# Kernel optimization log

Hardware: AMD Instinct MI355X
Metric: run time of the kernel (lower is better)

The kernel has to match this reference:

```python
import jax, jax.numpy as jnp
import numpy as np

B, T, IN, H, C = 128, 128, 75, 512, 60


def setup_inputs() -> dict:
    key = jax.random.key(0)
    ks = jax.random.split(key, 40)
    def n(k, shape, s=0.05):
        return jax.random.normal(k, shape, dtype=jnp.float32) * s
    p = {}
    p["inputs"] = jax.random.normal(ks[0], (B, T, IN), dtype=jnp.float32)
    p["epoch"] = 1
    # three used LSTMCells: lstm_cell_t, lstm_cell (spatial), lstm_cell1
    i = 1
    for nm, isz in [("t", IN), ("s", IN), ("1", IN)]:
        p[f"Wih_{nm}"] = n(ks[i], (4 * H, isz)); i += 1
        p[f"Whh_{nm}"] = n(ks[i], (4 * H, H)); i += 1
        p[f"bih_{nm}"] = n(ks[i], (4 * H,)); i += 1
        p[f"bhh_{nm}"] = n(ks[i], (4 * H,)); i += 1
    p["fc_w"] = n(ks[i], (C, H)); i += 1
    p["fc_b"] = n(ks[i], (C,)); i += 1
    p["fct_w"] = n(ks[i], (H, IN)); i += 1
    p["fct_b"] = n(ks[i], (H,)); i += 1
    p["fc1_w"] = n(ks[i], (H, IN)); i += 1
    p["fc1_b"] = n(ks[i], (H,)); i += 1
    p["fc2_w"] = n(ks[i], (IN // 3, H)); i += 1
    p["fc2_b"] = n(ks[i], (IN // 3,)); i += 1
    p["W_x_t"] = n(ks[i], (H, H)); i += 1
    p["W_h_t"] = n(ks[i], (H, H)); i += 1
    p["b_t"] = n(ks[i], (H,)); i += 1
    p["W_x_s"] = n(ks[i], (H, H)); i += 1
    p["W_h_s"] = n(ks[i], (H, H)); i += 1
    p["U_s"] = n(ks[i], (H, H)); i += 1
    p["b_s"] = n(ks[i], (H,)); i += 1
    p["b_us"] = n(ks[i], (H,)); i += 1
    return p


def reference(inputs, epoch,
              Wih_t, Whh_t, bih_t, bhh_t,
              Wih_s, Whh_s, bih_s, bhh_s,
              Wih_1, Whh_1, bih_1, bhh_1,
              fc_w, fc_b, fct_w, fct_b, fc1_w, fc1_b, fc2_w, fc2_b,
              W_x_t, W_h_t, b_t, W_x_s, W_h_s, U_s, b_s, b_us):
    def cell(x, h, c, Wih, Whh, bih, bhh):
        g = x @ Wih.T + bih + h @ Whh.T + bhh            # [B, 4H]
        i, f, gg, o = jnp.split(g, 4, axis=1)
        c2 = jax.nn.sigmoid(f) * c + jax.nn.sigmoid(i) * jnp.tanh(gg)
        return jax.nn.sigmoid(o) * jnp.tanh(c2), c2

    def step(carry, x):  # x: [B, IN]
        hn_t, cn_t, hn_s, cn_s, hn1, cn1 = carry
        h_prev_t = hn_t
        hn_t, cn_t = cell(x, hn_t, cn_t, Wih_t, Whh_t, bih_t, bhh_t)
        # temporal gate beta (note: original adds BOTH b_s and b_t)
        beta = jax.nn.relu((x @ fct_w.T + fct_b) @ W_x_t + h_prev_t @ W_h_t + b_s + b_t)
        h_prev = hn_s
        hn_s, cn_s = cell(x, hn_s, cn_s, Wih_s, Whh_s, bih_s, bhh_s)
        st = jnp.tanh((x @ fc1_w.T + fc1_b) @ W_x_s + h_prev @ W_h_s + b_s)
        st = st @ U_s + b_us
        q = st @ fc2_w.T + fc2_b                          # [B, IN/3]
        alpha = jax.nn.softmax(q, axis=1)                  # exp(q)/sum(exp(q))
        x_gated = x * jnp.repeat(alpha, 3, axis=1)
        hn1, cn1 = cell(x_gated, hn1, cn1, Wih_1, Whh_1, bih_1, bhh_1)
        # torch in-place aliasing bug: zt = hn1; zt *= beta mutates hn1,
        # so the gated value is carried as the next-step hidden state.
        hn1 = hn1 * beta
        return (hn_t, cn_t, hn_s, cn_s, hn1, cn1), (hn1, alpha, beta)

    Bn, Tn = inputs.shape[0], inputs.shape[1]
    z = jnp.zeros((Bn, Whh_t.shape[1]), dtype=inputs.dtype)
    init = (z, z, z, z, z, z)
    xs = jnp.swapaxes(inputs, 0, 1)  # [T, B, IN]
    _, (outs, alphas, betas) = jax.lax.scan(step, init, xs)
    logits = outs[-1] @ fc_w.T + fc_b
    logp = jax.nn.log_softmax(logits, axis=-1)
    # original reshapes the [T, B, *] stacks directly to (B, T, -1)
    alpha_out = alphas.reshape(Bn, Tn, -1)
    beta_out = betas.reshape(Bn, Tn, -1)
    return logp, alpha_out, beta_out
```

## Files before the change

kernel.cpp:

```cpp
#include <hip/hip_runtime.h>
#include <math.h>

#define B_ 128
#define T_ 128
#define IN_ 75
#define H_ 512
#define C_ 60
#define Q_ 25

constexpr size_t OFF_WHHP = 0;
constexpr size_t OFF_WIHP = 6291456;
constexpr size_t OFF_WXHP = 7225344;
constexpr size_t OFF_FT2P = 9322496;
constexpr size_t OFF_U2   = 9478144;
constexpr size_t OFF_B2   = 9529344;
constexpr size_t OFF_XP   = 9529472;
constexpr size_t OFF_HT2  = 12019840;
constexpr size_t OFF_HS2  = 12281984;
constexpr size_t OFF_T12  = 12544128;
constexpr size_t OFF_T22  = 12806272;
constexpr size_t OFF_H12  = 13068416;
constexpr size_t OFF_CT   = 13199488;
constexpr size_t OFF_CS   = 13461632;
constexpr size_t OFF_C1   = 13723776;
constexpr size_t OFF_G1H  = 13985920;
constexpr size_t OFF_ST   = 14510208;
constexpr size_t OFF_BETA = 14772352;
constexpr size_t WS_BYTES = 15034496;

struct Full {
  const float* inputs;
  const float* Wih_t; const float* Whh_t; const float* bih_t; const float* bhh_t;
  const float* Wih_s; const float* Whh_s; const float* bih_s; const float* bhh_s;
  const float* Wih_1; const float* Whh_1; const float* bih_1; const float* bhh_1;
  const float* fc_w;  const float* fc_b;
  const float* fct_w; const float* fct_b;
  const float* fc1_w; const float* fc1_b;
  const float* fc2_w; const float* fc2_b;
  const float* W_x_t; const float* W_h_t; const float* b_t;
  const float* W_x_s; const float* W_h_s; const float* U_s; const float* b_s; const float* b_us;
  char* ws; float* out;
};

typedef _Float16 h2t __attribute__((ext_vector_type(2)));
union U32H { unsigned u; h2t h; unsigned short s[2]; };

__device__ __forceinline__ float sigm(float v) { return 1.f / (1.f + expf(-v)); }
__device__ __forceinline__ float dot2(unsigned a, unsigned b, float c) {
#if __has_builtin(__builtin_amdgcn_fdot2)
  U32H A, B; A.u = a; B.u = b;
  return __builtin_amdgcn_fdot2(A.h, B.h, c, false);
#else
  U32H A, B; A.u = a; B.u = b;
  return fmaf((float)A.h.x, (float)B.h.x, fmaf((float)A.h.y, (float)B.h.y, c));
#endif
}
__device__ __forceinline__ unsigned pack2h(float a, float b) {
  U32H r; r.h.x = (_Float16)a; r.h.y = (_Float16)b; return r.u;
}
__device__ __forceinline__ float hlo(unsigned v) { U32H r; r.u = v; return (float)r.h.x; }
__device__ __forceinline__ float hhi(unsigned v) { U32H r; r.u = v; return (float)r.h.y; }

__global__ void prep_pack(Full f) {
  uint4* WHHP = (uint4*)(f.ws + OFF_WHHP);
  uint4* WIHP = (uint4*)(f.ws + OFF_WIHP);
  unsigned* WXHP = (unsigned*)(f.ws + OFF_WXHP);
  unsigned* FT2P = (unsigned*)(f.ws + OFF_FT2P);
  float* U2 = (float*)(f.ws + OFF_U2);
  float* B2 = (float*)(f.ws + OFF_B2);
  unsigned* XP = (unsigned*)(f.ws + OFF_XP);

  const size_t N1 = (size_t)3 * 256 * 512;
  const size_t N2 = (size_t)3 * 38 * 512;
  const size_t N3 = (size_t)4 * 256 * 512;
  const size_t N4 = (size_t)2 * 38 * 512;
  const size_t N5 = (size_t)25 * 512;
  const size_t N6 = 25;
  const size_t N7 = (size_t)128 * 38 * 128;
  const size_t TOT = N1 + N2 + N3 + N4 + N5 + N6 + N7;
  for (size_t i = (size_t)blockIdx.x * blockDim.x + threadIdx.x; i < TOT;
       i += (size_t)gridDim.x * blockDim.x) {
    if (i < N1) {
      size_t c = i / 131072, r = i % 131072, k2 = r >> 9, u = r & 511;
      const float* W = (c == 0) ? f.Whh_t : (c == 1) ? f.Whh_s : f.Whh_1;
      uint4 v;
      v.x = pack2h(W[(0 * 512 + u) * 512 + 2 * k2], W[(0 * 512 + u) * 512 + 2 * k2 + 1]);
      v.y = pack2h(W[(1 * 512 + u) * 512 + 2 * k2], W[(1 * 512 + u) * 512 + 2 * k2 + 1]);
      v.z = pack2h(W[(2 * 512 + u) * 512 + 2 * k2], W[(2 * 512 + u) * 512 + 2 * k2 + 1]);
      v.w = pack2h(W[(3 * 512 + u) * 512 + 2 * k2], W[(3 * 512 + u) * 512 + 2 * k2 + 1]);
      WHHP[i] = v;
    } else if (i < N1 + N2) {
      size_t e = i - N1; size_t c = e / 19456, r = e % 19456, k2 = r >> 9, u = r & 511;
      const float* W = (c == 0) ? f.Wih_t : (c == 1) ? f.Wih_s : f.Wih_1;
      int k = 2 * (int)k2;
      uint4 v;
#pragma unroll
      for (int g = 0; g < 4; ++g) {
        float a = (k < 75) ? W[(g * 512 + u) * 75 + k] : 0.f;
        float b = (k + 1 < 75) ? W[(g * 512 + u) * 75 + k + 1] : 0.f;
        (&v.x)[g] = pack2h(a, b);
      }
      WIHP[e] = v;
    } else if (i < N1 + N2 + N3) {
      size_t e = i - N1 - N2; size_t w = e / 131072, r = e % 131072, k2 = r >> 9, u = r & 511;
      const float* W = (w == 0) ? f.W_x_t : (w == 1) ? f.W_h_t : (w == 2) ? f.W_x_s : f.W_h_s;
      WXHP[e] = pack2h(W[2 * k2 * 512 + u], W[(2 * k2 + 1) * 512 + u]);
    } else if (i < N1 + N2 + N3 + N4) {
      size_t e = i - N1 - N2 - N3; size_t c = e / 19456, r = e % 19456, k2 = r >> 9, u = r & 511;
      const float* W = c ? f.fc1_w : f.fct_w;
      int k = 2 * (int)k2;
      float a = (k < 75) ? W[u * 75 + k] : 0.f;
      float b = (k + 1 < 75) ? W[u * 75 + k + 1] : 0.f;
      FT2P[e] = pack2h(a, b);
    } else if (i < N1 + N2 + N3 + N4 + N5) {
      size_t e = i - N1 - N2 - N3 - N4; size_t qi = e >> 9, u = e & 511;
      float acc = 0.f;
      for (int n = 0; n < 512; ++n) acc = fmaf(f.U_s[u * 512 + n], f.fc2_w[qi * 512 + n], acc);
      U2[qi * 512 + u] = acc;
    } else if (i < N1 + N2 + N3 + N4 + N5 + N6) {
      size_t qi = i - N1 - N2 - N3 - N4 - N5;
      float acc = f.fc2_b[qi];
      for (int n = 0; n < 512; ++n) acc = fmaf(f.b_us[n], f.fc2_w[qi * 512 + n], acc);
      B2[qi] = acc;
    } else {
      size_t e = i - N1 - N2 - N3 - N4 - N5 - N6;
      size_t t = e / 4864, r = e % 4864, k2 = r >> 7, b = r & 127;
      int k = 2 * (int)k2;
      const size_t base = ((size_t)b * T_ + t) * IN_;
      float xa = (k < 75) ? f.inputs[base + k] : 0.f;
      float xb = (k + 1 < 75) ? f.inputs[base + k + 1] : 0.f;
      XP[e] = pack2h(xa, xb);
    }
  }
}

__global__ __launch_bounds__(512) void prep_state(Full f) {
  const int b = blockIdx.x, j = threadIdx.x;
  __shared__ float x0[77];
  __shared__ float t1L[512], t2L[512];
  if (j < IN_) x0[j] = f.inputs[(size_t)b * T_ * IN_ + j];
  __syncthreads();
  float t1 = f.fct_b[j], t2 = f.fc1_b[j];
  for (int k = 0; k < IN_; ++k) {
    t1 = fmaf(x0[k], f.fct_w[j * IN_ + k], t1);
    t2 = fmaf(x0[k], f.fc1_w[j * IN_ + k], t2);
  }
  t1L[j] = t1; t2L[j] = t2;
  __syncthreads();
  ((float*)(f.ws + OFF_CT))[(size_t)j * 128 + b] = 0.f;
  ((float*)(f.ws + OFF_CS))[(size_t)j * 128 + b] = 0.f;
  ((float*)(f.ws + OFF_C1))[(size_t)j * 128 + b] = 0.f;
  if (j < 256) {
    ((unsigned*)(f.ws + OFF_HT2))[(size_t)j * 128 + b] = 0u;
    ((unsigned*)(f.ws + OFF_HS2))[(size_t)j * 128 + b] = 0u;
    ((unsigned*)(f.ws + OFF_H12))[(size_t)j * 128 + b] = 0u;
    ((unsigned*)(f.ws + OFF_T12))[(size_t)j * 128 + b] = pack2h(t1L[2 * j], t1L[2 * j + 1]);
    ((unsigned*)(f.ws + OFF_T22))[(size_t)j * 128 + b] = pack2h(t2L[2 * j], t2L[2 * j + 1]);
  }
}

__global__ __launch_bounds__(256) void k1(Full f, int t) {
  const int tid = threadIdx.x, bid = blockIdx.x;
  const int row = tid & 127, half = tid >> 7;
  const int cur = t & 1;

  char* wsb = f.ws;
  const uint4* WHHP = (const uint4*)(wsb + OFF_WHHP);
  const uint4* WIHP = (const uint4*)(wsb + OFF_WIHP);
  const unsigned* WXHP = (const unsigned*)(wsb + OFF_WXHP);
  const unsigned* FT2P = (const unsigned*)(wsb + OFF_FT2P);
  const unsigned* XP = (const unsigned*)(wsb + OFF_XP);
  unsigned* HT2 = (unsigned*)(wsb + OFF_HT2);
  unsigned* HS2 = (unsigned*)(wsb + OFF_HS2);
  unsigned* T12 = (unsigned*)(wsb + OFF_T12);
  unsigned* T22 = (unsigned*)(wsb + OFF_T22);
  unsigned* H12 = (unsigned*)(wsb + OFF_H12);
  float* CT = (float*)(wsb + OFF_CT);
  float* CS = (float*)(wsb + OFF_CS);
  uint4* G1H = (uint4*)(wsb + OFF_G1H);
  float* ST = (float*)(wsb + OFF_ST);
  float* BETA = (float*)(wsb + OFF_BETA);
  float* out_beta = f.out + B_ * C_ + (size_t)T_ * B_ * Q_;

  if (bid < 384) {
    const int c = bid / 128;
    const int up = (bid % 128) * 2 + half;
    const int u0 = 2 * up, u1 = u0 + 1;
    const unsigned* Sr = (c == 0) ? (HT2 + (size_t)cur * 32768)
                       : (c == 1) ? (HS2 + (size_t)cur * 32768) : H12;
    float a0 = 0, a1 = 0, a2 = 0, a3 = 0, a4 = 0, a5 = 0, a6 = 0, a7 = 0;
#pragma unroll 4
    for (int k2 = 0; k2 < 256; ++k2) {
      const unsigned s = Sr[k2 * 128 + row];
      const uint4 w0 = WHHP[((size_t)(c * 256 + k2) << 9) + u0];
      const uint4 w1 = WHHP[((size_t)(c * 256 + k2) << 9) + u1];
      a0 = dot2(s, w0.x, a0); a1 = dot2(s, w0.y, a1);
      a2 = dot2(s, w0.z, a2); a3 = dot2(s, w0.w, a3);
      a4 = dot2(s, w1.x, a4); a5 = dot2(s, w1.y, a5);
      a6 = dot2(s, w1.z, a6); a7 = dot2(s, w1.w, a7);
    }
    if (c < 2) {
#pragma unroll 2
      for (int k2 = 0; k2 < 38; ++k2) {
        const unsigned xp = XP[((size_t)t * 38 + k2) * 128 + row];
        const uint4 w0 = WIHP[((size_t)(c * 38 + k2) << 9) + u0];
        const uint4 w1 = WIHP[((size_t)(c * 38 + k2) << 9) + u1];
        a0 = dot2(xp, w0.x, a0); a1 = dot2(xp, w0.y, a1);
        a2 = dot2(xp, w0.z, a2); a3 = dot2(xp, w0.w, a3);
        a4 = dot2(xp, w1.x, a4); a5 = dot2(xp, w1.y, a5);
        a6 = dot2(xp, w1.z, a6); a7 = dot2(xp, w1.w, a7);
      }
      const float* bi = c ? f.bih_s : f.bih_t;
      const float* bh = c ? f.bhh_s : f.bhh_t;
      float* Cst = c ? CS : CT;
      float h0, h1v;
      {
        const float iv = sigm(a0 + bi[u0] + bh[u0]);
        const float fv = sigm(a1 + bi[512 + u0] + bh[512 + u0]);
        const float gv = tanhf(a2 + bi[1024 + u0] + bh[1024 + u0]);
        const float ov = sigm(a3 + bi[1536 + u0] + bh[1536 + u0]);
        const float cc = fv * Cst[(size_t)u0 * 128 + row] + iv * gv;
        Cst[(size_t)u0 * 128 + row] = cc;
        h0 = ov * tanhf(cc);
      }
      {
        const float iv = sigm(a4 + bi[u1] + bh[u1]);
        const float fv = sigm(a5 + bi[512 + u1] + bh[512 + u1]);
        const float gv = tanhf(a6 + bi[1024 + u1] + bh[1024 + u1]);
        const float ov = sigm(a7 + bi[1536 + u1] + bh[1536 + u1]);
        const float cc = fv * Cst[(size_t)u1 * 128 + row] + iv * gv;
        Cst[(size_t)u1 * 128 + row] = cc;
        h1v = ov * tanhf(cc);
      }
      unsigned* Sw = (c ? HS2 : HT2) + (size_t)(cur ^ 1) * 32768;
      Sw[up * 128 + row] = pack2h(h0, h1v);
    } else {
      uint4 g;
      g.x = pack2h(a0 + f.bih_1[u0] + f.bhh_1[u0], a4 + f.bih_1[u1] + f.bhh_1[u1]);
      g.y = pack2h(a1 + f.bih_1[512 + u0] + f.bhh_1[512 + u0],
                   a5 + f.bih_1[512 + u1] + f.bhh_1[512 + u1]);
      g.z = pack2h(a2 + f.bih_1[1024 + u0] + f.bhh_1[1024 + u0],
                   a6 + f.bih_1[1024 + u1] + f.bhh_1[1024 + u1]);
      g.w = pack2h(a3 + f.bih_1[1536 + u0] + f.bhh_1[1536 + u0],
                   a7 + f.bih_1[1536 + u1] + f.bhh_1[1536 + u1]);
      G1H[(size_t)up * 128 + row] = g;
    }
  } else if (bid < 512) {
    const int up = (bid - 384) * 2 + half;
    const int u0 = 2 * up, u1 = u0 + 1;
    const unsigned* T1r = T12 + (size_t)cur * 32768;
    const unsigned* HTr = HT2 + (size_t)cur * 32768;
    float aB0 = 0, aB1 = 0;
#pragma unroll 4
    for (int k2 = 0; k2 < 256; ++k2) {
      const unsigned t1 = T1r[k2 * 128 + row];
      const unsigned ht = HTr[k2 * 128 + row];
      aB0 = dot2(t1, WXHP[((size_t)k2 << 9) + u0], aB0);
      aB0 = dot2(ht, WXHP[((size_t)(256 + k2) << 9) + u0], aB0);
      aB1 = dot2(t1, WXHP[((size_t)k2 << 9) + u1], aB1);
      aB1 = dot2(ht, WXHP[((size_t)(256 + k2) << 9) + u1], aB1);
    }
    {
      const float bv = fmaxf(aB0 + f.b_s[u0] + f.b_t[u0], 0.f);
      BETA[(size_t)u0 * 128 + row] = bv;
      out_beta[((size_t)t * B_ + row) * H_ + u0] = bv;
    }
    {
      const float bv = fmaxf(aB1 + f.b_s[u1] + f.b_t[u1], 0.f);
      BETA[(size_t)u1 * 128 + row] = bv;
      out_beta[((size_t)t * B_ + row) * H_ + u1] = bv;
    }
    if (t < T_ - 1) {
      float tn0 = 0, tn1 = 0;
#pragma unroll 2
      for (int k2 = 0; k2 < 38; ++k2) {
        const unsigned xp = XP[((size_t)(t + 1) * 38 + k2) * 128 + row];
        tn0 = dot2(xp, FT2P[((size_t)k2 << 9) + u0], tn0);
        tn1 = dot2(xp, FT2P[((size_t)k2 << 9) + u1], tn1);
      }
      T12[(size_t)(cur ^ 1) * 32768 + up * 128 + row] =
          pack2h(tn0 + f.fct_b[u0], tn1 + f.fct_b[u1]);
    }
  } else {
    const int up = (bid - 512) * 2 + half;
    const int u0 = 2 * up, u1 = u0 + 1;
    const unsigned* T2r = T22 + (size_t)cur * 32768;
    const unsigned* HSr = HS2 + (size_t)cur * 32768;
    float aS0 = 0, aS1 = 0;
#pragma unroll 4
    for (int k2 = 0; k2 < 256; ++k2) {
      const unsigned t2 = T2r[k2 * 128 + row];
      const unsigned hs = HSr[k2 * 128 + row];
      aS0 = dot2(t2, WXHP[((size_t)(512 + k2) << 9) + u0], aS0);
      aS0 = dot2(hs, WXHP[((size_t)(768 + k2) << 9) + u0], aS0);
      aS1 = dot2(t2, WXHP[((size_t)(512 + k2) << 9) + u1], aS1);
      aS1 = dot2(hs, WXHP[((size_t)(768 + k2) << 9) + u1], aS1);
    }
    ST[(size_t)u0 * 128 + row] = tanhf(aS0 + f.b_s[u0]);
    ST[(size_t)u1 * 128 + row] = tanhf(aS1 + f.b_s[u1]);
    if (t < T_ - 1) {
      float tn0 = 0, tn1 = 0;
#pragma unroll 2
      for (int k2 = 0; k2 < 38; ++k2) {
        const unsigned xp = XP[((size_t)(t + 1) * 38 + k2) * 128 + row];
        tn0 = dot2(xp, FT2P[((size_t)(38 + k2) << 9) + u0], tn0);
        tn1 = dot2(xp, FT2P[((size_t)(38 + k2) << 9) + u1], tn1);
      }
      T22[(size_t)(cur ^ 1) * 32768 + up * 128 + row] =
          pack2h(tn0 + f.fc1_b[u0], tn1 + f.fc1_b[u1]);
    }
  }
}

__global__ __launch_bounds__(256) void k2(Full f, int t) {
  const int tid = threadIdx.x, row = blockIdx.x;
  char* wsb = f.ws;
  const uint4* WIHP = (const uint4*)(wsb + OFF_WIHP);
  const float* U2 = (const float*)(wsb + OFF_U2);
  const float* B2 = (const float*)(wsb + OFF_B2);
  const float* ST = (const float*)(wsb + OFF_ST);
  const float* BETA = (const float*)(wsb + OFF_BETA);
  const uint4* G1H = (const uint4*)(wsb + OFF_G1H);
  float* C1 = (float*)(wsb + OFF_C1);
  unsigned* H12 = (unsigned*)(wsb + OFF_H12);
  float* out_alpha = f.out + B_ * C_;

  __shared__ float stv[512];
  __shared__ float qp[200];
  __shared__ float qv[25];
  __shared__ float al[25];
  __shared__ unsigned xgp[40];

  stv[tid] = ST[(size_t)tid * 128 + row];
  stv[tid + 256] = ST[(size_t)(tid + 256) * 128 + row];
  __syncthreads();
  if (tid < 200) {
    const int qi = tid >> 3, ks = tid & 7;
    const float* u2p = U2 + (size_t)qi * 512 + ks * 64;
    const float* sp = stv + ks * 64;
    float acc = 0.f;
    for (int j = 0; j < 64; j += 4) {
      const float4 uv = *(const float4*)(u2p + j);
      const float4 sv = *(const float4*)(sp + j);
      acc += sv.x * uv.x + sv.y * uv.y + sv.z * uv.z + sv.w * uv.w;
    }
    qp[tid] = acc;
  }
  __syncthreads();
  if (tid < 25) {
    float s = B2[tid];
    for (int j = 0; j < 8; ++j) s += qp[tid * 8 + j];
    qv[tid] = s;
  }
  __syncthreads();
  if (tid < 25) {
    float m = qv[0];
    for (int i2 = 1; i2 < 25; ++i2) m = fmaxf(m, qv[i2]);
    float s = 0.f;
    for (int i2 = 0; i2 < 25; ++i2) s += expf(qv[i2] - m);
    const float a = expf(qv[tid] - m) / s;
    al[tid] = a;
    out_alpha[((size_t)t * B_ + row) * Q_ + tid] = a;
  }
  __syncthreads();
  if (tid < 38) {
    const int k = 2 * tid;
    const size_t base = ((size_t)row * T_ + t) * IN_;
    const float xa = f.inputs[base + k] * al[k / 3];
    const float xb = (k + 1 < IN_) ? f.inputs[base + k + 1] * al[(k + 1) / 3] : 0.f;
    xgp[tid] = pack2h(xa, xb);
  }
  __syncthreads();
  const int u0 = 2 * tid, u1 = u0 + 1;
  float c0 = 0, c1a = 0, c2 = 0, c3 = 0, c4 = 0, c5 = 0, c6 = 0, c7 = 0;
#pragma unroll 2
  for (int k2 = 0; k2 < 38; ++k2) {
    const unsigned xp = xgp[k2];
    const uint4 w0 = WIHP[((size_t)(2 * 38 + k2) << 9) + u0];
    const uint4 w1 = WIHP[((size_t)(2 * 38 + k2) << 9) + u1];
    c0 = dot2(xp, w0.x, c0); c1a = dot2(xp, w0.y, c1a);
    c2 = dot2(xp, w0.z, c2); c3 = dot2(xp, w0.w, c3);
    c4 = dot2(xp, w1.x, c4); c5 = dot2(xp, w1.y, c5);
    c6 = dot2(xp, w1.z, c6); c7 = dot2(xp, w1.w, c7);
  }
  const uint4 g = G1H[(size_t)tid * 128 + row];
  float h0, h1v;
  {
    const float i1 = sigm(c0 + hlo(g.x)), f1 = sigm(c1a + hlo(g.y));
    const float gg = tanhf(c2 + hlo(g.z)), o1 = sigm(c3 + hlo(g.w));
    const float cc = f1 * C1[(size_t)u0 * 128 + row] + i1 * gg;
    C1[(size_t)u0 * 128 + row] = cc;
    h0 = o1 * tanhf(cc) * BETA[(size_t)u0 * 128 + row];
  }
  {
    const float i1 = sigm(c4 + hhi(g.x)), f1 = sigm(c5 + hhi(g.y));
    const float gg = tanhf(c6 + hhi(g.z)), o1 = sigm(c7 + hhi(g.w));
    const float cc = f1 * C1[(size_t)u1 * 128 + row] + i1 * gg;
    C1[(size_t)u1 * 128 + row] = cc;
    h1v = o1 * tanhf(cc) * BETA[(size_t)u1 * 128 + row];
  }
  H12[(size_t)tid * 128 + row] = pack2h(h0, h1v);
}

__global__ __launch_bounds__(256) void k3(Full f) {
  const int tid = threadIdx.x, row = blockIdx.x;
  const unsigned* H12 = (const unsigned*)(f.ws + OFF_H12);
  __shared__ float hv[512];
  __shared__ float part[240];
  __shared__ float lg[60];
  {
    const unsigned v = H12[(size_t)tid * 128 + row];
    hv[2 * tid] = hlo(v);
    hv[2 * tid + 1] = hhi(v);
  }
  __syncthreads();
  if (tid < 240) {
    const int ci = tid >> 2, ks = tid & 3;
    const float* fr = f.fc_w + (size_t)ci * 512 + ks * 128;
    const float* hr = hv + ks * 128;
    float acc = 0.f;
    for (int j = 0; j < 128; j += 4) {
      const float4 fv = *(const float4*)(fr + j);
      const float4 hq = *(const float4*)(hr + j);
      acc += hq.x * fv.x + hq.y * fv.y + hq.z * fv.z + hq.w * fv.w;
    }
    part[tid] = acc;
  }
  __syncthreads();
  if (tid < 60) {
    float s = f.fc_b[tid];
    for (int j = 0; j < 4; ++j) s += part[tid * 4 + j];
    lg[tid] = s;
  }
  __syncthreads();
  if (tid < 60) {
    float m = lg[0];
    for (int i2 = 1; i2 < 60; ++i2) m = fmaxf(m, lg[i2]);
    float ssum = 0.f;
    for (int i2 = 0; i2 < 60; ++i2) ssum += expf(lg[i2] - m);
    f.out[(size_t)row * C_ + tid] = lg[tid] - m - logf(ssum);
  }
}

extern "C" void kernel_launch(void* const* d_in, const int* in_sizes, int n_in,
                              void* d_out, int out_size, void* d_ws, size_t ws_size,
                              hipStream_t stream) {
  if (ws_size < WS_BYTES) return;

  Full f;
  f.inputs = (const float*)d_in[0];
  f.Wih_t = (const float*)d_in[2];  f.Whh_t = (const float*)d_in[3];
  f.bih_t = (const float*)d_in[4];  f.bhh_t = (const float*)d_in[5];
  f.Wih_s = (const float*)d_in[6];  f.Whh_s = (const float*)d_in[7];
  f.bih_s = (const float*)d_in[8];  f.bhh_s = (const float*)d_in[9];
  f.Wih_1 = (const float*)d_in[10]; f.Whh_1 = (const float*)d_in[11];
  f.bih_1 = (const float*)d_in[12]; f.bhh_1 = (const float*)d_in[13];
  f.fc_w  = (const float*)d_in[14]; f.fc_b  = (const float*)d_in[15];
  f.fct_w = (const float*)d_in[16]; f.fct_b = (const float*)d_in[17];
  f.fc1_w = (const float*)d_in[18]; f.fc1_b = (const float*)d_in[19];
  f.fc2_w = (const float*)d_in[20]; f.fc2_b = (const float*)d_in[21];
  f.W_x_t = (const float*)d_in[22]; f.W_h_t = (const float*)d_in[23];
  f.b_t   = (const float*)d_in[24];
  f.W_x_s = (const float*)d_in[25]; f.W_h_s = (const float*)d_in[26];
  f.U_s   = (const float*)d_in[27]; f.b_s   = (const float*)d_in[28];
  f.b_us  = (const float*)d_in[29];
  f.ws = (char*)d_ws;
  f.out = (float*)d_out;

  hipLaunchKernelGGL(prep_pack, dim3(1024), dim3(256), 0, stream, f);
  hipLaunchKernelGGL(prep_state, dim3(128), dim3(512), 0, stream, f);

  for (int t = 0; t < T_; ++t) {
    hipLaunchKernelGGL(k1, dim3(640), dim3(256), 0, stream, f, t);
    hipLaunchKernelGGL(k2, dim3(128), dim3(256), 0, stream, f, t);
  }
  hipLaunchKernelGGL(k3, dim3(128), dim3(256), 0, stream, f);
}
```

Measured before the change: 9.808 ms.

## Replace per-timestep kernel launches with one persistent batch-parallel scan kernel

The 256 per-step launches of k1/k2 are replaced by a single scanB kernel where each of 64 blocks owns two batch rows and runs all 128 timesteps, keeping hidden and cell states in shared memory and registers. All three LSTM cells, the beta and spatial-attention matmuls, the input projections and the final FC/log-softmax are fused into this loop. Weight packing is reorganised so each thread streams its gate columns as uint4 per step. This removes launch overhead and global state round-trips, but every block re-reads the full fp16 weight set (about 8 MB) from L2/HBM on every step, and only 64 blocks occupy the GPU.

```diff
diff --git a/kernel.cpp b/kernel.cpp
--- a/kernel.cpp
+++ b/kernel.cpp
@@ -8,25 +8,18 @@
 #define C_ 60
 #define Q_ 25
 
-constexpr size_t OFF_WHHP = 0;
-constexpr size_t OFF_WIHP = 6291456;
-constexpr size_t OFF_WXHP = 7225344;
-constexpr size_t OFF_FT2P = 9322496;
-constexpr size_t OFF_U2   = 9478144;
-constexpr size_t OFF_B2   = 9529344;
-constexpr size_t OFF_XP   = 9529472;
-constexpr size_t OFF_HT2  = 12019840;
-constexpr size_t OFF_HS2  = 12281984;
-constexpr size_t OFF_T12  = 12544128;
-constexpr size_t OFF_T22  = 12806272;
-constexpr size_t OFF_H12  = 13068416;
-constexpr size_t OFF_CT   = 13199488;
-constexpr size_t OFF_CS   = 13461632;
-constexpr size_t OFF_C1   = 13723776;
-constexpr size_t OFF_G1H  = 13985920;
-constexpr size_t OFF_ST   = 14510208;
-constexpr size_t OFF_BETA = 14772352;
-constexpr size_t WS_BYTES = 15034496;
+constexpr size_t OFF_WHH3 = 0;
+constexpr size_t SZ_WHH3  = 3ull * 256 * 512 * 16;
+constexpr size_t OFF_WX4  = OFF_WHH3 + SZ_WHH3;
+constexpr size_t SZ_WX4   = 256ull * 512 * 16;
+constexpr size_t OFF_WIH3 = OFF_WX4 + SZ_WX4;
+constexpr size_t SZ_WIH3  = 3ull * 38 * 512 * 16;
+constexpr size_t OFF_FT2  = OFF_WIH3 + SZ_WIH3;
+constexpr size_t SZ_FT2   = 38ull * 512 * 8;
+constexpr size_t OFF_U2   = OFF_FT2 + SZ_FT2;
+constexpr size_t SZ_U2    = 25ull * 512 * 4;
+constexpr size_t OFF_B2   = OFF_U2 + SZ_U2;
+constexpr size_t WS_BYTES = OFF_B2 + 128;
 
 struct Full {
   const float* inputs;
@@ -58,39 +51,47 @@
 __device__ __forceinline__ unsigned pack2h(float a, float b) {
   U32H r; r.h.x = (_Float16)a; r.h.y = (_Float16)b; return r.u;
 }
+__device__ __forceinline__ unsigned short f2h(float a) {
+  U32H r; r.u = 0; r.h.x = (_Float16)a; return r.s[0];
+}
 __device__ __forceinline__ float hlo(unsigned v) { U32H r; r.u = v; return (float)r.h.x; }
 __device__ __forceinline__ float hhi(unsigned v) { U32H r; r.u = v; return (float)r.h.y; }
 
 __global__ void prep_pack(Full f) {
-  uint4* WHHP = (uint4*)(f.ws + OFF_WHHP);
-  uint4* WIHP = (uint4*)(f.ws + OFF_WIHP);
-  unsigned* WXHP = (unsigned*)(f.ws + OFF_WXHP);
-  unsigned* FT2P = (unsigned*)(f.ws + OFF_FT2P);
+  uint4* WHH3 = (uint4*)(f.ws + OFF_WHH3);
+  uint4* WX4 = (uint4*)(f.ws + OFF_WX4);
+  uint4* WIH3 = (uint4*)(f.ws + OFF_WIH3);
+  uint2* FT2 = (uint2*)(f.ws + OFF_FT2);
   float* U2 = (float*)(f.ws + OFF_U2);
   float* B2 = (float*)(f.ws + OFF_B2);
-  unsigned* XP = (unsigned*)(f.ws + OFF_XP);
-
-  const size_t N1 = (size_t)3 * 256 * 512;
-  const size_t N2 = (size_t)3 * 38 * 512;
-  const size_t N3 = (size_t)4 * 256 * 512;
-  const size_t N4 = (size_t)2 * 38 * 512;
-  const size_t N5 = (size_t)25 * 512;
+
+  const size_t N1 = 3ull * 256 * 512;
+  const size_t N2 = 256ull * 512;
+  const size_t N3 = 3ull * 38 * 512;
+  const size_t N4 = 38ull * 512;
+  const size_t N5 = 25ull * 512;
   const size_t N6 = 25;
-  const size_t N7 = (size_t)128 * 38 * 128;
-  const size_t TOT = N1 + N2 + N3 + N4 + N5 + N6 + N7;
+  const size_t TOT = N1 + N2 + N3 + N4 + N5 + N6;
   for (size_t i = (size_t)blockIdx.x * blockDim.x + threadIdx.x; i < TOT;
        i += (size_t)gridDim.x * blockDim.x) {
     if (i < N1) {
       size_t c = i / 131072, r = i % 131072, k2 = r >> 9, u = r & 511;
       const float* W = (c == 0) ? f.Whh_t : (c == 1) ? f.Whh_s : f.Whh_1;
       uint4 v;
-      v.x = pack2h(W[(0 * 512 + u) * 512 + 2 * k2], W[(0 * 512 + u) * 512 + 2 * k2 + 1]);
-      v.y = pack2h(W[(1 * 512 + u) * 512 + 2 * k2], W[(1 * 512 + u) * 512 + 2 * k2 + 1]);
-      v.z = pack2h(W[(2 * 512 + u) * 512 + 2 * k2], W[(2 * 512 + u) * 512 + 2 * k2 + 1]);
-      v.w = pack2h(W[(3 * 512 + u) * 512 + 2 * k2], W[(3 * 512 + u) * 512 + 2 * k2 + 1]);
-      WHHP[i] = v;
+#pragma unroll
+      for (int g = 0; g < 4; ++g)
+        (&v.x)[g] = pack2h(W[(g * 512 + u) * 512 + 2 * k2], W[(g * 512 + u) * 512 + 2 * k2 + 1]);
+      WHH3[i] = v;
     } else if (i < N1 + N2) {
-      size_t e = i - N1; size_t c = e / 19456, r = e % 19456, k2 = r >> 9, u = r & 511;
+      size_t e = i - N1, k2 = e >> 9, u = e & 511;
+      uint4 v;
+      v.x = pack2h(f.W_x_t[2 * k2 * 512 + u], f.W_x_t[(2 * k2 + 1) * 512 + u]);
+      v.y = pack2h(f.W_h_t[2 * k2 * 512 + u], f.W_h_t[(2 * k2 + 1) * 512 + u]);
+      v.z = pack2h(f.W_x_s[2 * k2 * 512 + u], f.W_x_s[(2 * k2 + 1) * 512 + u]);
+      v.w = pack2h(f.W_h_s[2 * k2 * 512 + u], f.W_h_s[(2 * k2 + 1) * 512 + u]);
+      WX4[e] = v;
+    } else if (i < N1 + N2 + N3) {
+      size_t e = i - N1 - N2, c = e / 19456, r = e % 19456, k2 = r >> 9, u = r & 511;
       const float* W = (c == 0) ? f.Wih_t : (c == 1) ? f.Wih_s : f.Wih_1;
       int k = 2 * (int)k2;
       uint4 v;
@@ -100,345 +101,315 @@
         float b = (k + 1 < 75) ? W[(g * 512 + u) * 75 + k + 1] : 0.f;
         (&v.x)[g] = pack2h(a, b);
       }
-      WIHP[e] = v;
-    } else if (i < N1 + N2 + N3) {
-      size_t e = i - N1 - N2; size_t w = e / 131072, r = e % 131072, k2 = r >> 9, u = r & 511;
-      const float* W = (w == 0) ? f.W_x_t : (w == 1) ? f.W_h_t : (w == 2) ? f.W_x_s : f.W_h_s;
-      WXHP[e] = pack2h(W[2 * k2 * 512 + u], W[(2 * k2 + 1) * 512 + u]);
+      WIH3[e] = v;
     } else if (i < N1 + N2 + N3 + N4) {
-      size_t e = i - N1 - N2 - N3; size_t c = e / 19456, r = e % 19456, k2 = r >> 9, u = r & 511;
-      const float* W = c ? f.fc1_w : f.fct_w;
+      size_t e = i - N1 - N2 - N3, k2 = e >> 9, u = e & 511;
       int k = 2 * (int)k2;
-      float a = (k < 75) ? W[u * 75 + k] : 0.f;
-      float b = (k + 1 < 75) ? W[u * 75 + k + 1] : 0.f;
-      FT2P[e] = pack2h(a, b);
+      uint2 v;
+      {
+        float a = (k < 75) ? f.fct_w[u * 75 + k] : 0.f;
+        float b = (k + 1 < 75) ? f.fct_w[u * 75 + k + 1] : 0.f;
+        v.x = pack2h(a, b);
+      }
+      {
+        float a = (k < 75) ? f.fc1_w[u * 75 + k] : 0.f;
+        float b = (k + 1 < 75) ? f.fc1_w[u * 75 + k + 1] : 0.f;
+        v.y = pack2h(a, b);
+      }
+      FT2[e] = v;
     } else if (i < N1 + N2 + N3 + N4 + N5) {
-      size_t e = i - N1 - N2 - N3 - N4; size_t qi = e >> 9, u = e & 511;
+      size_t e = i - N1 - N2 - N3 - N4, qi = e >> 9, u = e & 511;
       float acc = 0.f;
       for (int n = 0; n < 512; ++n) acc = fmaf(f.U_s[u * 512 + n], f.fc2_w[qi * 512 + n], acc);
       U2[qi * 512 + u] = acc;
-    } else if (i < N1 + N2 + N3 + N4 + N5 + N6) {
+    } else {
       size_t qi = i - N1 - N2 - N3 - N4 - N5;
       float acc = f.fc2_b[qi];
       for (int n = 0; n < 512; ++n) acc = fmaf(f.b_us[n], f.fc2_w[qi * 512 + n], acc);
       B2[qi] = acc;
-    } else {
-      size_t e = i - N1 - N2 - N3 - N4 - N5 - N6;
-      size_t t = e / 4864, r = e % 4864, k2 = r >> 7, b = r & 127;
-      int k = 2 * (int)k2;
-      const size_t base = ((size_t)b * T_ + t) * IN_;
-      float xa = (k < 75) ? f.inputs[base + k] : 0.f;
-      float xb = (k + 1 < 75) ? f.inputs[base + k + 1] : 0.f;
-      XP[e] = pack2h(xa, xb);
-    }
-  }
-}
-
-__global__ __launch_bounds__(512) void prep_state(Full f) {
-  const int b = blockIdx.x, j = threadIdx.x;
-  __shared__ float x0[77];
-  __shared__ float t1L[512], t2L[512];
-  if (j < IN_) x0[j] = f.inputs[(size_t)b * T_ * IN_ + j];
+    }
+  }
+}
+
+__global__ __launch_bounds__(512, 2) void scanB(Full f) {
+  const int tid = threadIdx.x;
+  const int blk = blockIdx.x;
+  const int r0 = blk * 2;
+
+  const uint4* WHH3 = (const uint4*)(f.ws + OFF_WHH3);
+  const uint4* WX4 = (const uint4*)(f.ws + OFF_WX4);
+  const uint4* WIH3 = (const uint4*)(f.ws + OFF_WIH3);
+  const uint2* FT2 = (const uint2*)(f.ws + OFF_FT2);
+  const float* U2 = (const float*)(f.ws + OFF_U2);
+  const float* B2 = (const float*)(f.ws + OFF_B2);
+
+  float* out_logp = f.out;
+  float* out_alpha = f.out + B_ * C_;
+  float* out_beta = f.out + B_ * C_ + (size_t)T_ * B_ * Q_;
+
+  __shared__ unsigned short hT[2][2][512], hS[2][2][512], h1h[2][2][512];
+  __shared__ unsigned short t1h[2][2][512], t2h[2][2][512];
+  __shared__ unsigned xp[2][2][40], xg[2][40];
+  __shared__ float stf[2][512];
+  __shared__ float qp[2][25][8];
+  __shared__ float qv[2][32], al[2][32];
+  __shared__ float pl[2][60][4];
+  __shared__ float lg[2][64];
+
+  const float btb0 = f.bih_t[tid] + f.bhh_t[tid];
+  const float btb1 = f.bih_t[512 + tid] + f.bhh_t[512 + tid];
+  const float btb2 = f.bih_t[1024 + tid] + f.bhh_t[1024 + tid];
+  const float btb3 = f.bih_t[1536 + tid] + f.bhh_t[1536 + tid];
+  const float bsb0 = f.bih_s[tid] + f.bhh_s[tid];
+  const float bsb1 = f.bih_s[512 + tid] + f.bhh_s[512 + tid];
+  const float bsb2 = f.bih_s[1024 + tid] + f.bhh_s[1024 + tid];
+  const float bsb3 = f.bih_s[1536 + tid] + f.bhh_s[1536 + tid];
+  const float b1b0 = f.bih_1[tid] + f.bhh_1[tid];
+  const float b1b1 = f.bih_1[512 + tid] + f.bhh_1[512 + tid];
+  const float b1b2 = f.bih_1[1024 + tid] + f.bhh_1[1024 + tid];
+  const float b1b3 = f.bih_1[1536 + tid] + f.bhh_1[1536 + tid];
+  const float bB = f.b_s[tid] + f.b_t[tid];
+  const float bS = f.b_s[tid];
+  const float bT1 = f.fct_b[tid], bT2 = f.fc1_b[tid];
+
+  hT[0][0][tid] = 0; hT[0][1][tid] = 0;
+  hS[0][0][tid] = 0; hS[0][1][tid] = 0;
+  h1h[0][0][tid] = 0; h1h[0][1][tid] = 0;
+  if (tid < 76) {
+    const int rr = tid / 38, k2 = tid - rr * 38, k = 2 * k2;
+    const float* xb = f.inputs + ((size_t)(r0 + rr) * T_) * IN_;
+    const float xa = (k < 75) ? xb[k] : 0.f;
+    const float xv = (k + 1 < 75) ? xb[k + 1] : 0.f;
+    xp[0][rr][k2] = pack2h(xa, xv);
+  }
   __syncthreads();
-  float t1 = f.fct_b[j], t2 = f.fc1_b[j];
-  for (int k = 0; k < IN_; ++k) {
-    t1 = fmaf(x0[k], f.fct_w[j * IN_ + k], t1);
-    t2 = fmaf(x0[k], f.fc1_w[j * IN_ + k], t2);
-  }
-  t1L[j] = t1; t2L[j] = t2;
+  {
+    float t10 = bT1, t20 = bT2, t11 = bT1, t21 = bT2;
+    for (int k2 = 0; k2 < 38; ++k2) {
+      const uint2 ft = FT2[(size_t)k2 * 512 + tid];
+      const unsigned x0 = xp[0][0][k2], x1 = xp[0][1][k2];
+      t10 = dot2(x0, ft.x, t10); t20 = dot2(x0, ft.y, t20);
+      t11 = dot2(x1, ft.x, t11); t21 = dot2(x1, ft.y, t21);
+    }
+    t1h[0][0][tid] = f2h(t10); t1h[0][1][tid] = f2h(t11);
+    t2h[0][0][tid] = f2h(t20); t2h[0][1][tid] = f2h(t21);
+  }
   __syncthreads();
-  ((float*)(f.ws + OFF_CT))[(size_t)j * 128 + b] = 0.f;
-  ((float*)(f.ws + OFF_CS))[(size_t)j * 128 + b] = 0.f;
-  ((float*)(f.ws + OFF_C1))[(size_t)j * 128 + b] = 0.f;
-  if (j < 256) {
-    ((unsigned*)(f.ws + OFF_HT2))[(size_t)j * 128 + b] = 0u;
-    ((unsigned*)(f.ws + OFF_HS2))[(size_t)j * 128 + b] = 0u;
-    ((unsigned*)(f.ws + OFF_H12))[(size_t)j * 128 + b] = 0u;
-    ((unsigned*)(f.ws + OFF_T12))[(size_t)j * 128 + b] = pack2h(t1L[2 * j], t1L[2 * j + 1]);
-    ((unsigned*)(f.ws + OFF_T22))[(size_t)j * 128 + b] = pack2h(t2L[2 * j], t2L[2 * j + 1]);
-  }
-}
-
-__global__ __launch_bounds__(256) void k1(Full f, int t) {
-  const int tid = threadIdx.x, bid = blockIdx.x;
-  const int row = tid & 127, half = tid >> 7;
-  const int cur = t & 1;
-
-  char* wsb = f.ws;
-  const uint4* WHHP = (const uint4*)(wsb + OFF_WHHP);
-  const uint4* WIHP = (const uint4*)(wsb + OFF_WIHP);
-  const unsigned* WXHP = (const unsigned*)(wsb + OFF_WXHP);
-  const unsigned* FT2P = (const unsigned*)(wsb + OFF_FT2P);
-  const unsigned* XP = (const unsigned*)(wsb + OFF_XP);
-  unsigned* HT2 = (unsigned*)(wsb + OFF_HT2);
-  unsigned* HS2 = (unsigned*)(wsb + OFF_HS2);
-  unsigned* T12 = (unsigned*)(wsb + OFF_T12);
-  unsigned* T22 = (unsigned*)(wsb + OFF_T22);
-  unsigned* H12 = (unsigned*)(wsb + OFF_H12);
-  float* CT = (float*)(wsb + OFF_CT);
-  float* CS = (float*)(wsb + OFF_CS);
-  uint4* G1H = (uint4*)(wsb + OFF_G1H);
-  float* ST = (float*)(wsb + OFF_ST);
-  float* BETA = (float*)(wsb + OFF_BETA);
-  float* out_beta = f.out + B_ * C_ + (size_t)T_ * B_ * Q_;
-
-  if (bid < 384) {
-    const int c = bid / 128;
-    const int up = (bid % 128) * 2 + half;
-    const int u0 = 2 * up, u1 = u0 + 1;
-    const unsigned* Sr = (c == 0) ? (HT2 + (size_t)cur * 32768)
-                       : (c == 1) ? (HS2 + (size_t)cur * 32768) : H12;
-    float a0 = 0, a1 = 0, a2 = 0, a3 = 0, a4 = 0, a5 = 0, a6 = 0, a7 = 0;
-#pragma unroll 4
-    for (int k2 = 0; k2 < 256; ++k2) {
-      const unsigned s = Sr[k2 * 128 + row];
-      const uint4 w0 = WHHP[((size_t)(c * 256 + k2) << 9) + u0];
-      const uint4 w1 = WHHP[((size_t)(c * 256 + k2) << 9) + u1];
-      a0 = dot2(s, w0.x, a0); a1 = dot2(s, w0.y, a1);
-      a2 = dot2(s, w0.z, a2); a3 = dot2(s, w0.w, a3);
-      a4 = dot2(s, w1.x, a4); a5 = dot2(s, w1.y, a5);
-      a6 = dot2(s, w1.z, a6); a7 = dot2(s, w1.w, a7);
-    }
-    if (c < 2) {
+
+  float c_t0 = 0, c_t1 = 0, c_s0 = 0, c_s1 = 0, c10 = 0, c11 = 0;
+
+  for (int t = 0; t < T_; ++t) {
+    const int cur = t & 1, nxt = cur ^ 1;
+    float aT00 = 0, aT01 = 0, aT02 = 0, aT03 = 0, aT10 = 0, aT11 = 0, aT12 = 0, aT13 = 0;
+    float aS00 = 0, aS01 = 0, aS02 = 0, aS03 = 0, aS10 = 0, aS11 = 0, aS12 = 0, aS13 = 0;
+    float g00 = 0, g01 = 0, g02 = 0, g03 = 0, g10 = 0, g11 = 0, g12 = 0, g13 = 0;
+    float aB0 = 0, aB1 = 0, aQ0 = 0, aQ1 = 0;
+    {
+      const unsigned* hT0 = (const unsigned*)hT[cur][0];
+      const unsigned* hT1 = (const unsigned*)hT[cur][1];
+      const unsigned* hS0 = (const unsigned*)hS[cur][0];
+      const unsigned* hS1 = (const unsigned*)hS[cur][1];
+      const unsigned* h10 = (const unsigned*)h1h[cur][0];
+      const unsigned* h11 = (const unsigned*)h1h[cur][1];
+      const unsigned* t10p = (const unsigned*)t1h[cur][0];
+      const unsigned* t11p = (const unsigned*)t1h[cur][1];
+      const unsigned* t20p = (const unsigned*)t2h[cur][0];
+      const unsigned* t21p = (const unsigned*)t2h[cur][1];
+#pragma unroll 2
+      for (int k2 = 0; k2 < 256; ++k2) {
+        const uint4 wt = WHH3[(size_t)k2 * 512 + tid];
+        const uint4 wsv = WHH3[(size_t)(256 + k2) * 512 + tid];
+        const uint4 w1v = WHH3[(size_t)(512 + k2) * 512 + tid];
+        const uint4 wx = WX4[(size_t)k2 * 512 + tid];
+        const unsigned sT0 = hT0[k2], sT1 = hT1[k2];
+        const unsigned sS0 = hS0[k2], sS1 = hS1[k2];
+        const unsigned s10 = h10[k2], s11 = h11[k2];
+        const unsigned v10 = t10p[k2], v11 = t11p[k2];
+        const unsigned v20 = t20p[k2], v21 = t21p[k2];
+        aT00 = dot2(sT0, wt.x, aT00); aT01 = dot2(sT0, wt.y, aT01);
+        aT02 = dot2(sT0, wt.z, aT02); aT03 = dot2(sT0, wt.w, aT03);
+        aT10 = dot2(sT1, wt.x, aT10); aT11 = dot2(sT1, wt.y, aT11);
+        aT12 = dot2(sT1, wt.z, aT12); aT13 = dot2(sT1, wt.w, aT13);
+        aS00 = dot2(sS0, wsv.x, aS00); aS01 = dot2(sS0, wsv.y, aS01);
+        aS02 = dot2(sS0, wsv.z, aS02); aS03 = dot2(sS0, wsv.w, aS03);
+        aS10 = dot2(sS1, wsv.x, aS10); aS11 = dot2(sS1, wsv.y, aS11);
+        aS12 = dot2(sS1, wsv.z, aS12); aS13 = dot2(sS1, wsv.w, aS13);
+        g00 = dot2(s10, w1v.x, g00); g01 = dot2(s10, w1v.y, g01);
+        g02 = dot2(s10, w1v.z, g02); g03 = dot2(s10, w1v.w, g03);
+        g10 = dot2(s11, w1v.x, g10); g11 = dot2(s11, w1v.y, g11);
+        g12 = dot2(s11, w1v.z, g12); g13 = dot2(s11, w1v.w, g13);
+        aB0 = dot2(v10, wx.x, aB0); aB0 = dot2(sT0, wx.y, aB0);
+        aB1 = dot2(v11, wx.x, aB1); aB1 = dot2(sT1, wx.y, aB1);
+        aQ0 = dot2(v20, wx.z, aQ0); aQ0 = dot2(sS0, wx.w, aQ0);
+        aQ1 = dot2(v21, wx.z, aQ1); aQ1 = dot2(sS1, wx.w, aQ1);
+      }
+    }
+#pragma unroll 2
+    for (int k2 = 0; k2 < 38; ++k2) {
+      const uint4 wiT = WIH3[(size_t)k2 * 512 + tid];
+      const uint4 wiS = WIH3[(size_t)(38 + k2) * 512 + tid];
+      const unsigned x0 = xp[cur][0][k2], x1 = xp[cur][1][k2];
+      aT00 = dot2(x0, wiT.x, aT00); aT01 = dot2(x0, wiT.y, aT01);
+      aT02 = dot2(x0, wiT.z, aT02); aT03 = dot2(x0, wiT.w, aT03);
+      aT10 = dot2(x1, wiT.x, aT10); aT11 = dot2(x1, wiT.y, aT11);
+      aT12 = dot2(x1, wiT.z, aT12); aT13 = dot2(x1, wiT.w, aT13);
+      aS00 = dot2(x0, wiS.x, aS00); aS01 = dot2(x0, wiS.y, aS01);
+      aS02 = dot2(x0, wiS.z, aS02); aS03 = dot2(x0, wiS.w, aS03);
+      aS10 = dot2(x1, wiS.x, aS10); aS11 = dot2(x1, wiS.y, aS11);
+      aS12 = dot2(x1, wiS.z, aS12); aS13 = dot2(x1, wiS.w, aS13);
+    }
+    {
+      const float iv = sigm(aT00 + btb0), fv = sigm(aT01 + btb1);
+      const float gv = tanhf(aT02 + btb2), ov = sigm(aT03 + btb3);
+      c_t0 = fv * c_t0 + iv * gv;
+      hT[nxt][0][tid] = f2h(ov * tanhf(c_t0));
+    }
+    {
+      const float iv = sigm(aT10 + btb0), fv = sigm(aT11 + btb1);
+      const float gv = tanhf(aT12 + btb2), ov = sigm(aT13 + btb3);
+      c_t1 = fv * c_t1 + iv * gv;
+      hT[nxt][1][tid] = f2h(ov * tanhf(c_t1));
+    }
+    {
+      const float iv = sigm(aS00 + bsb0), fv = sigm(aS01 + bsb1);
+      const float gv = tanhf(aS02 + bsb2), ov = sigm(aS03 + bsb3);
+      c_s0 = fv * c_s0 + iv * gv;
+      hS[nxt][0][tid] = f2h(ov * tanhf(c_s0));
+    }
+    {
+      const float iv = sigm(aS10 + bsb0), fv = sigm(aS11 + bsb1);
+      const float gv = tanhf(aS12 + bsb2), ov = sigm(aS13 + bsb3);
+      c_s1 = fv * c_s1 + iv * gv;
+      hS[nxt][1][tid] = f2h(ov * tanhf(c_s1));
+    }
+    const float bta0 = fmaxf(aB0 + bB, 0.f);
+    const float bta1 = fmaxf(aB1 + bB, 0.f);
+    out_beta[((size_t)t * B_ + r0) * H_ + tid] = bta0;
+    out_beta[((size_t)t * B_ + r0 + 1) * H_ + tid] = bta1;
+    stf[0][tid] = tanhf(aQ0 + bS);
+    stf[1][tid] = tanhf(aQ1 + bS);
+    const float gh00 = g00 + b1b0, gh01 = g01 + b1b1, gh02 = g02 + b1b2, gh03 = g03 + b1b3;
+    const float gh10 = g10 + b1b0, gh11 = g11 + b1b1, gh12 = g12 + b1b2, gh13 = g13 + b1b3;
+    __syncthreads();
+
+    {
+      const int rr = tid >> 8, rem = tid & 255;
+      if (rem < 200) {
+        const int qi = rem >> 3, ks = rem & 7;
+        const float* u2p = U2 + (size_t)qi * 512 + ks * 64;
+        const float* sp = &stf[rr][ks * 64];
+        float acc = 0.f;
+        for (int j = 0; j < 64; j += 4) {
+          const float4 uv = *(const float4*)(u2p + j);
+          const float4 sv = *(const float4*)(sp + j);
+          acc += sv.x * uv.x + sv.y * uv.y + sv.z * uv.z + sv.w * uv.w;
+        }
+        qp[rr][qi][ks] = acc;
+      }
+    }
+    __syncthreads();
+    {
+      const int rr = tid >> 8, rem = tid & 255;
+      if (rem < 25) {
+        float s = B2[rem];
+#pragma unroll
+        for (int j = 0; j < 8; ++j) s += qp[rr][rem][j];
+        qv[rr][rem] = s;
+      }
+    }
+    __syncthreads();
+    {
+      const int rr = tid >> 8, rem = tid & 255;
+      if (rem < 25) {
+        float m = qv[rr][0];
+        for (int i2 = 1; i2 < 25; ++i2) m = fmaxf(m, qv[rr][i2]);
+        float s = 0.f;
+        for (int i2 = 0; i2 < 25; ++i2) s += expf(qv[rr][i2] - m);
+        const float a = expf(qv[rr][rem] - m) / s;
+        al[rr][rem] = a;
+        out_alpha[((size_t)t * B_ + r0 + rr) * Q_ + rem] = a;
+      }
+    }
+    __syncthreads();
+
+    if (tid < 76) {
+      const int rr = tid / 38, k2 = tid - rr * 38, k = 2 * k2;
+      const unsigned xv = xp[cur][rr][k2];
+      const float ga = hlo(xv) * al[rr][k / 3];
+      const float gb = (k + 1 < IN_) ? hhi(xv) * al[rr][(k + 1) / 3] : 0.f;
+      xg[rr][k2] = pack2h(ga, gb);
+      if (t < T_ - 1) {
+        const float* xb = f.inputs + ((size_t)(r0 + rr) * T_ + t + 1) * IN_;
+        const float xa = (k < 75) ? xb[k] : 0.f;
+        const float xc = (k + 1 < 75) ? xb[k + 1] : 0.f;
+        xp[nxt][rr][k2] = pack2h(xa, xc);
+      }
+    }
+    __syncthreads();
+
+    if (t < T_ - 1) {
+      float t10 = bT1, t20 = bT2, t11 = bT1, t21 = bT2;
+      for (int k2 = 0; k2 < 38; ++k2) {
+        const uint2 ft = FT2[(size_t)k2 * 512 + tid];
+        const unsigned x0 = xp[nxt][0][k2], x1 = xp[nxt][1][k2];
+        t10 = dot2(x0, ft.x, t10); t20 = dot2(x0, ft.y, t20);
+        t11 = dot2(x1, ft.x, t11); t21 = dot2(x1, ft.y, t21);
+      }
+      t1h[nxt][0][tid] = f2h(t10); t1h[nxt][1][tid] = f2h(t11);
+      t2h[nxt][0][tid] = f2h(t20); t2h[nxt][1][tid] = f2h(t21);
+    }
+    {
+      float cx00 = 0, cx01 = 0, cx02 = 0, cx03 = 0, cx10 = 0, cx11 = 0, cx12 = 0, cx13 = 0;
 #pragma unroll 2
       for (int k2 = 0; k2 < 38; ++k2) {
-        const unsigned xp = XP[((size_t)t * 38 + k2) * 128 + row];
-        const uint4 w0 = WIHP[((size_t)(c * 38 + k2) << 9) + u0];
-        const uint4 w1 = WIHP[((size_t)(c * 38 + k2) << 9) + u1];
-        a0 = dot2(xp, w0.x, a0); a1 = dot2(xp, w0.y, a1);
-        a2 = dot2(xp, w0.z, a2); a3 = dot2(xp, w0.w, a3);
-        a4 = dot2(xp, w1.x, a4); a5 = dot2(xp, w1.y, a5);
-        a6 = dot2(xp, w1.z, a6); a7 = dot2(xp, w1.w, a7);
-      }
-      const float* bi = c ? f.bih_s : f.bih_t;
-      const float* bh = c ? f.bhh_s : f.bhh_t;
-      float* Cst = c ? CS : CT;
-      float h0, h1v;
+        const uint4 w1 = WIH3[(size_t)(76 + k2) * 512 + tid];
+        const unsigned x0 = xg[0][k2], x1 = xg[1][k2];
+        cx00 = dot2(x0, w1.x, cx00); cx01 = dot2(x0, w1.y, cx01);
+        cx02 = dot2(x0, w1.z, cx02); cx03 = dot2(x0, w1.w, cx03);
+        cx10 = dot2(x1, w1.x, cx10); cx11 = dot2(x1, w1.y, cx11);
+        cx12 = dot2(x1, w1.z, cx12); cx13 = dot2(x1, w1.w, cx13);
+      }
       {
-        const float iv = sigm(a0 + bi[u0] + bh[u0]);
-        const float fv = sigm(a1 + bi[512 + u0] + bh[512 + u0]);
-        const float gv = tanhf(a2 + bi[1024 + u0] + bh[1024 + u0]);
-        const float ov = sigm(a3 + bi[1536 + u0] + bh[1536 + u0]);
-        const float cc = fv * Cst[(size_t)u0 * 128 + row] + iv * gv;
-        Cst[(size_t)u0 * 128 + row] = cc;
-        h0 = ov * tanhf(cc);
+        const float i1 = sigm(cx00 + gh00), f1 = sigm(cx01 + gh01);
+        const float gg = tanhf(cx02 + gh02), o1 = sigm(cx03 + gh03);
+        c10 = f1 * c10 + i1 * gg;
+        h1h[nxt][0][tid] = f2h(o1 * tanhf(c10) * bta0);
       }
       {
-        const float iv = sigm(a4 + bi[u1] + bh[u1]);
-        const float fv = sigm(a5 + bi[512 + u1] + bh[512 + u1]);
-        const float gv = tanhf(a6 + bi[1024 + u1] + bh[1024 + u1]);
-        const float ov = sigm(a7 + bi[1536 + u1] + bh[1536 + u1]);
-        const float cc = fv * Cst[(size_t)u1 * 128 + row] + iv * gv;
-        Cst[(size_t)u1 * 128 + row] = cc;
-        h1v = ov * tanhf(cc);
-      }
-      unsigned* Sw = (c ? HS2 : HT2) + (size_t)(cur ^ 1) * 32768;
-      Sw[up * 128 + row] = pack2h(h0, h1v);
-    } else {
-      uint4 g;
-      g.x = pack2h(a0 + f.bih_1[u0] + f.bhh_1[u0], a4 + f.bih_1[u1] + f.bhh_1[u1]);
-      g.y = pack2h(a1 + f.bih_1[512 + u0] + f.bhh_1[512 + u0],
-                   a5 + f.bih_1[512 + u1] + f.bhh_1[512 + u1]);
-      g.z = pack2h(a2 + f.bih_1[1024 + u0] + f.bhh_1[1024 + u0],
-                   a6 + f.bih_1[1024 + u1] + f.bhh_1[1024 + u1]);
-      g.w = pack2h(a3 + f.bih_1[1536 + u0] + f.bhh_1[1536 + u0],
-                   a7 + f.bih_1[1536 + u1] + f.bhh_1[1536 + u1]);
-      G1H[(size_t)up * 128 + row] = g;
-    }
-  } else if (bid < 512) {
-    const int up = (bid - 384) * 2 + half;
-    const int u0 = 2 * up, u1 = u0 + 1;
-    const unsigned* T1r = T12 + (size_t)cur * 32768;
-    const unsigned* HTr = HT2 + (size_t)cur * 32768;
-    float aB0 = 0, aB1 = 0;
-#pragma unroll 4
-    for (int k2 = 0; k2 < 256; ++k2) {
-      const unsigned t1 = T1r[k2 * 128 + row];
-      const unsigned ht = HTr[k2 * 128 + row];
-      aB0 = dot2(t1, WXHP[((size_t)k2 << 9) + u0], aB0);
-      aB0 = dot2(ht, WXHP[((size_t)(256 + k2) << 9) + u0], aB0);
-      aB1 = dot2(t1, WXHP[((size_t)k2 << 9) + u1], aB1);
-      aB1 = dot2(ht, WXHP[((size_t)(256 + k2) << 9) + u1], aB1);
-    }
-    {
-      const float bv = fmaxf(aB0 + f.b_s[u0] + f.b_t[u0], 0.f);
-      BETA[(size_t)u0 * 128 + row] = bv;
-      out_beta[((size_t)t * B_ + row) * H_ + u0] = bv;
-    }
-    {
-      const float bv = fmaxf(aB1 + f.b_s[u1] + f.b_t[u1], 0.f);
-      BETA[(size_t)u1 * 128 + row] = bv;
-      out_beta[((size_t)t * B_ + row) * H_ + u1] = bv;
-    }
-    if (t < T_ - 1) {
-      float tn0 = 0, tn1 = 0;
-#pragma unroll 2
-      for (int k2 = 0; k2 < 38; ++k2) {
-        const unsigned xp = XP[((size_t)(t + 1) * 38 + k2) * 128 + row];
-        tn0 = dot2(xp, FT2P[((size_t)k2 << 9) + u0], tn0);
-        tn1 = dot2(xp, FT2P[((size_t)k2 << 9) + u1], tn1);
-      }
-      T12[(size_t)(cur ^ 1) * 32768 + up * 128 + row] =
-          pack2h(tn0 + f.fct_b[u0], tn1 + f.fct_b[u1]);
-    }
-  } else {
-    const int up = (bid - 512) * 2 + half;
-    const int u0 = 2 * up, u1 = u0 + 1;
-    const unsigned* T2r = T22 + (size_t)cur * 32768;
-    const unsigned* HSr = HS2 + (size_t)cur * 32768;
-    float aS0 = 0, aS1 = 0;
-#pragma unroll 4
-    for (int k2 = 0; k2 < 256; ++k2) {
-      const unsigned t2 = T2r[k2 * 128 + row];
-      const unsigned hs = HSr[k2 * 128 + row];
-      aS0 = dot2(t2, WXHP[((size_t)(512 + k2) << 9) + u0], aS0);
-      aS0 = dot2(hs, WXHP[((size_t)(768 + k2) << 9) + u0], aS0);
-      aS1 = dot2(t2, WXHP[((size_t)(512 + k2) << 9) + u1], aS1);
-      aS1 = dot2(hs, WXHP[((size_t)(768 + k2) << 9) + u1], aS1);
-    }
-    ST[(size_t)u0 * 128 + row] = tanhf(aS0 + f.b_s[u0]);
-    ST[(size_t)u1 * 128 + row] = tanhf(aS1 + f.b_s[u1]);
-    if (t < T_ - 1) {
-      float tn0 = 0, tn1 = 0;
-#pragma unroll 2
-      for (int k2 = 0; k2 < 38; ++k2) {
-        const unsigned xp = XP[((size_t)(t + 1) * 38 + k2) * 128 + row];
-        tn0 = dot2(xp, FT2P[((size_t)(38 + k2) << 9) + u0], tn0);
-        tn1 = dot2(xp, FT2P[((size_t)(38 + k2) << 9) + u1], tn1);
-      }
-      T22[(size_t)(cur ^ 1) * 32768 + up * 128 + row] =
-          pack2h(tn0 + f.fc1_b[u0], tn1 + f.fc1_b[u1]);
-    }
-  }
-}
-
-__global__ __launch_bounds__(256) void k2(Full f, int t) {
-  const int tid = threadIdx.x, row = blockIdx.x;
-  char* wsb = f.ws;
-  const uint4* WIHP = (const uint4*)(wsb + OFF_WIHP);
-  const float* U2 = (const float*)(wsb + OFF_U2);
-  const float* B2 = (const float*)(wsb + OFF_B2);
-  const float* ST = (const float*)(wsb + OFF_ST);
-  const float* BETA = (const float*)(wsb + OFF_BETA);
-  const uint4* G1H = (const uint4*)(wsb + OFF_G1H);
-  float* C1 = (float*)(wsb + OFF_C1);
-  unsigned* H12 = (unsigned*)(wsb + OFF_H12);
-  float* out_alpha = f.out + B_ * C_;
-
-  __shared__ float stv[512];
-  __shared__ float qp[200];
-  __shared__ float qv[25];
-  __shared__ float al[25];
-  __shared__ unsigned xgp[40];
-
-  stv[tid] = ST[(size_t)tid * 128 + row];
-  stv[tid + 256] = ST[(size_t)(tid + 256) * 128 + row];
+        const float i1 = sigm(cx10 + gh10), f1 = sigm(cx11 + gh11);
+        const float gg = tanhf(cx12 + gh12), o1 = sigm(cx13 + gh13);
+        c11 = f1 * c11 + i1 * gg;
+        h1h[nxt][1][tid] = f2h(o1 * tanhf(c11) * bta1);
+      }
+    }
+    __syncthreads();
+  }
+
+  if (tid < 480) {
+    const int rr = tid / 240, rem = tid % 240, ci = rem >> 2, ks = rem & 3;
+    const float* fr = f.fc_w + (size_t)ci * 512 + ks * 128;
+    const unsigned* hp = (const unsigned*)h1h[0][rr];
+    float acc = 0.f;
+    for (int e = 0; e < 64; ++e) {
+      const unsigned v = hp[ks * 64 + e];
+      acc = fmaf(hlo(v), fr[2 * e], acc);
+      acc = fmaf(hhi(v), fr[2 * e + 1], acc);
+    }
+    pl[rr][ci][ks] = acc;
+  }
   __syncthreads();
-  if (tid < 200) {
-    const int qi = tid >> 3, ks = tid & 7;
-    const float* u2p = U2 + (size_t)qi * 512 + ks * 64;
-    const float* sp = stv + ks * 64;
-    float acc = 0.f;
-    for (int j = 0; j < 64; j += 4) {
-      const float4 uv = *(const float4*)(u2p + j);
-      const float4 sv = *(const float4*)(sp + j);
-      acc += sv.x * uv.x + sv.y * uv.y + sv.z * uv.z + sv.w * uv.w;
-    }
-    qp[tid] = acc;
+  if (tid < 120) {
+    const int rr = tid / 60, ci = tid % 60;
+    lg[rr][ci] = f.fc_b[ci] + pl[rr][ci][0] + pl[rr][ci][1] + pl[rr][ci][2] + pl[rr][ci][3];
   }
   __syncthreads();
-  if (tid < 25) {
-    float s = B2[tid];
-    for (int j = 0; j < 8; ++j) s += qp[tid * 8 + j];
-    qv[tid] = s;
-  }
-  __syncthreads();
-  if (tid < 25) {
-    float m = qv[0];
-    for (int i2 = 1; i2 < 25; ++i2) m = fmaxf(m, qv[i2]);
+  if (tid < 120) {
+    const int rr = tid / 60, ci = tid % 60;
+    float m = lg[rr][0];
+    for (int i2 = 1; i2 < 60; ++i2) m = fmaxf(m, lg[rr][i2]);
     float s = 0.f;
-    for (int i2 = 0; i2 < 25; ++i2) s += expf(qv[i2] - m);
-    const float a = expf(qv[tid] - m) / s;
-    al[tid] = a;
-    out_alpha[((size_t)t * B_ + row) * Q_ + tid] = a;
-  }
-  __syncthreads();
-  if (tid < 38) {
-    const int k = 2 * tid;
-    const size_t base = ((size_t)row * T_ + t) * IN_;
-    const float xa = f.inputs[base + k] * al[k / 3];
-    const float xb = (k + 1 < IN_) ? f.inputs[base + k + 1] * al[(k + 1) / 3] : 0.f;
-    xgp[tid] = pack2h(xa, xb);
-  }
-  __syncthreads();
-  const int u0 = 2 * tid, u1 = u0 + 1;
-  float c0 = 0, c1a = 0, c2 = 0, c3 = 0, c4 = 0, c5 = 0, c6 = 0, c7 = 0;
-#pragma unroll 2
-  for (int k2 = 0; k2 < 38; ++k2) {
-    const unsigned xp = xgp[k2];
-    const uint4 w0 = WIHP[((size_t)(2 * 38 + k2) << 9) + u0];
-    const uint4 w1 = WIHP[((size_t)(2 * 38 + k2) << 9) + u1];
-    c0 = dot2(xp, w0.x, c0); c1a = dot2(xp, w0.y, c1a);
-    c2 = dot2(xp, w0.z, c2); c3 = dot2(xp, w0.w, c3);
-    c4 = dot2(xp, w1.x, c4); c5 = dot2(xp, w1.y, c5);
-    c6 = dot2(xp, w1.z, c6); c7 = dot2(xp, w1.w, c7);
-  }
-  const uint4 g = G1H[(size_t)tid * 128 + row];
-  float h0, h1v;
-  {
-    const float i1 = sigm(c0 + hlo(g.x)), f1 = sigm(c1a + hlo(g.y));
-    const float gg = tanhf(c2 + hlo(g.z)), o1 = sigm(c3 + hlo(g.w));
-    const float cc = f1 * C1[(size_t)u0 * 128 + row] + i1 * gg;
-    C1[(size_t)u0 * 128 + row] = cc;
-    h0 = o1 * tanhf(cc) * BETA[(size_t)u0 * 128 + row];
-  }
-  {
-    const float i1 = sigm(c4 + hhi(g.x)), f1 = sigm(c5 + hhi(g.y));
-    const float gg = tanhf(c6 + hhi(g.z)), o1 = sigm(c7 + hhi(g.w));
-    const float cc = f1 * C1[(size_t)u1 * 128 + row] + i1 * gg;
-    C1[(size_t)u1 * 128 + row] = cc;
-    h1v = o1 * tanhf(cc) * BETA[(size_t)u1 * 128 + row];
-  }
-  H12[(size_t)tid * 128 + row] = pack2h(h0, h1v);
-}
-
-__global__ __launch_bounds__(256) void k3(Full f) {
-  const int tid = threadIdx.x, row = blockIdx.x;
-  const unsigned* H12 = (const unsigned*)(f.ws + OFF_H12);
-  __shared__ float hv[512];
-  __shared__ float part[240];
-  __shared__ float lg[60];
-  {
-    const unsigned v = H12[(size_t)tid * 128 + row];
-    hv[2 * tid] = hlo(v);
-    hv[2 * tid + 1] = hhi(v);
-  }
-  __syncthreads();
-  if (tid < 240) {
-    const int ci = tid >> 2, ks = tid & 3;
-    const float* fr = f.fc_w + (size_t)ci * 512 + ks * 128;
-    const float* hr = hv + ks * 128;
-    float acc = 0.f;
-    for (int j = 0; j < 128; j += 4) {
-      const float4 fv = *(const float4*)(fr + j);
-      const float4 hq = *(const float4*)(hr + j);
-      acc += hq.x * fv.x + hq.y * fv.y + hq.z * fv.z + hq.w * fv.w;
-    }
-    part[tid] = acc;
-  }
-  __syncthreads();
-  if (tid < 60) {
-    float s = f.fc_b[tid];
-    for (int j = 0; j < 4; ++j) s += part[tid * 4 + j];
-    lg[tid] = s;
-  }
-  __syncthreads();
-  if (tid < 60) {
-    float m = lg[0];
-    for (int i2 = 1; i2 < 60; ++i2) m = fmaxf(m, lg[i2]);
-    float ssum = 0.f;
-    for (int i2 = 0; i2 < 60; ++i2) ssum += expf(lg[i2] - m);
-    f.out[(size_t)row * C_ + tid] = lg[tid] - m - logf(ssum);
+    for (int i2 = 0; i2 < 60; ++i2) s += expf(lg[rr][i2] - m);
+    out_logp[(size_t)(r0 + rr) * C_ + ci] = lg[rr][ci] - m - logf(s);
   }
 }
 
@@ -467,12 +438,6 @@
   f.ws = (char*)d_ws;
   f.out = (float*)d_out;
 
-  hipLaunchKernelGGL(prep_pack, dim3(1024), dim3(256), 0, stream, f);
-  hipLaunchKernelGGL(prep_state, dim3(128), dim3(512), 0, stream, f);
-
-  for (int t = 0; t < T_; ++t) {
-    hipLaunchKernelGGL(k1, dim3(640), dim3(256), 0, stream, f, t);
-    hipLaunchKernelGGL(k2, dim3(128), dim3(256), 0, stream, f, t);
-  }
-  hipLaunchKernelGGL(k3, dim3(128), dim3(256), 0, stream, f);
-}
+  hipLaunchKernelGGL(prep_pack, dim3(512), dim3(256), 0, stream, f);
+  hipLaunchKernelGGL(scanB, dim3(64), dim3(512), 0, stream, f);
+}
```

Result: slower. 12.09 ms (+23.3%).
